# Kernel optimization log

Measured on AMD Instinct MI355X. Metric: run time of the kernel, lower is better.

The kernel has to match this reference:

```python
import jax, jax.numpy as jnp
import numpy as np

N_NODES = 50000
N_EDGES = 800000
IN_CH, OUT_CH, HEADS = 64, 32, 4
NEG_SLOPE = 0.2
BN_EPS = 1e-5


def setup_inputs() -> dict:
    key = jax.random.key(0)
    ks = jax.random.split(key, 9)
    x = jax.random.normal(ks[0], (N_NODES, IN_CH), dtype=jnp.float32)
    pos = jax.random.uniform(ks[1], (N_NODES, 3), dtype=jnp.float32)
    edge_index = jax.random.randint(ks[2], (2, N_EDGES), 0, N_NODES, dtype=jnp.int64)
    s = 1.0 / np.sqrt(IN_CH)
    W_l = jax.random.normal(ks[3], (IN_CH, HEADS * OUT_CH), dtype=jnp.float32) * s
    W_r = jax.random.normal(ks[4], (IN_CH, HEADS * OUT_CH), dtype=jnp.float32) * s
    W_edge = jax.random.normal(ks[5], (3, HEADS * OUT_CH), dtype=jnp.float32) * 0.5
    att = jax.random.normal(ks[6], (HEADS, OUT_CH), dtype=jnp.float32) * (1.0 / np.sqrt(OUT_CH))
    bn_gamma = jax.random.uniform(ks[7], (HEADS * OUT_CH,), dtype=jnp.float32, minval=0.5, maxval=1.5)
    bn_beta = jax.random.normal(ks[8], (HEADS * OUT_CH,), dtype=jnp.float32) * 0.1
    return {"x": x, "pos": pos, "edge_index": edge_index, "W_l": W_l, "W_r": W_r,
            "W_edge": W_edge, "att": att, "bn_gamma": bn_gamma, "bn_beta": bn_beta}


def reference(x, pos, edge_index, W_l, W_r, W_edge, att, bn_gamma, bn_beta):
    N = x.shape[0]
    H, C = att.shape
    # source->target projections (GATv2: lin_l for source/messages, lin_r for target)
    xl = (x @ W_l).reshape(N, H, C)
    xr = (x @ W_r).reshape(N, H, C)
    src, dst = edge_index[0], edge_index[1]
    edge_attr = pos[src] - pos[dst]  # [E,3] relative position as edge feature
    # add self-loops with fill_value='mean' (PyG default)
    loop = jnp.arange(N)
    src = jnp.concatenate([src, loop])
    dst = jnp.concatenate([dst, loop])
    mean_attr = edge_attr.mean(axis=0, keepdims=True)  # [1,3]
    edge_attr = jnp.concatenate([edge_attr, jnp.broadcast_to(mean_attr, (N, 3))], axis=0)
    # per-edge GATv2 score: att . LeakyReLU(x_l[j] + x_r[i] + W_e e_ij)
    e_feat = (edge_attr @ W_edge).reshape(-1, H, C)
    msg = xl[src]                              # [Et,H,C] (reused for aggregation)
    e = msg + xr[dst] + e_feat
    e = jax.nn.leaky_relu(e, NEG_SLOPE)
    score = jnp.einsum('ehc,hc->eh', e, att)   # [Et,H]
    # segment softmax over destination node
    m = jax.ops.segment_max(score, dst, num_segments=N)
    score = jnp.exp(score - m[dst])
    denom = jax.ops.segment_sum(score, dst, num_segments=N)
    alpha = score / (denom[dst] + 1e-16)       # [Et,H]
    out = jax.ops.segment_sum(alpha[:, :, None] * msg, dst, num_segments=N)
    out = out.reshape(N, H * C)
    # BatchNorm over node dimension (training-mode batch statistics, PyG BatchNorm)
    mu = out.mean(axis=0)
    var = out.var(axis=0)
    return (out - mu) / jnp.sqrt(var + BN_EPS) * bn_gamma + bn_beta
```

## Files before the change

kernel.cpp:

```cpp
#include <hip/hip_runtime.h>
#include <hip/hip_bf16.h>

#define N_NODES 50000
#define IN_CH 64
#define HC 128
#define CAP 64
#define NEG_SLOPE 0.2f
#define BN_EPS 1e-5f


__global__ __launch_bounds__(256) void k_gemm(const float* __restrict__ x,
                                              const float* __restrict__ Wl,
                                              const float* __restrict__ Wr,
                                              unsigned int* __restrict__ xl_bf,
                                              float* __restrict__ xr_out,
                                              int* __restrict__ deg,
                                              float* __restrict__ mean_sums,
                                              float* __restrict__ bn_sums,
                                              int* __restrict__ flag,
                                              const int* __restrict__ eidx) {
  {
    int gtid = blockIdx.x * 256 + threadIdx.x;
    if (gtid < N_NODES) deg[gtid] = 1;
    if (gtid < 256) bn_sums[gtid] = 0.f;
    if (gtid < 3) mean_sums[gtid] = 0.f;
    if (blockIdx.x == 0 && threadIdx.x < 64) {
      int w = eidx[2 * threadIdx.x + 1];
      unsigned long long nz = __ballot(w != 0);
      if (threadIdx.x == 0) flag[0] = (nz == 0ULL) ? 1 : 0;
    }
  }

  __shared__ float xs[16][IN_CH];
  __shared__ __hip_bfloat162 wsm[IN_CH][128];
  const int t = threadIdx.x;
  const int row0 = blockIdx.x * 16;

  for (int i = 0; i < 32; ++i) {
    int k = i * 2 + (t >> 7);
    int p = t & 127;
    int cc = p * 2;
    float2 wv;
    if (cc < 128) wv = *(const float2*)(Wl + k * 128 + cc);
    else          wv = *(const float2*)(Wr + k * 128 + (cc - 128));
    wsm[k][p] = __float22bfloat162_rn(wv);
  }
  {
    int r = t >> 4, c4 = (t & 15) * 4;
    *(float4*)&xs[r][c4] = *(const float4*)(x + (row0 + r) * IN_CH + c4);
  }
  __syncthreads();

  const int ct = t & 63;
  const int rt = t >> 6;
  const int c4 = ct * 4;
  const int r4 = rt * 4;

  float acc[4][4];
  #pragma unroll
  for (int a = 0; a < 4; ++a)
    #pragma unroll
    for (int b = 0; b < 4; ++b) acc[a][b] = 0.f;

  #pragma unroll 8
  for (int k = 0; k < IN_CH; ++k) {
    uint2 wraw = *(const uint2*)&wsm[k][ct * 2];
    float2 f01 = __bfloat1622float2(*(__hip_bfloat162*)&wraw.x);
    float2 f23 = __bfloat1622float2(*(__hip_bfloat162*)&wraw.y);
    float wv[4] = {f01.x, f01.y, f23.x, f23.y};
    float xv[4] = {xs[r4][k], xs[r4 + 1][k], xs[r4 + 2][k], xs[r4 + 3][k]};
    #pragma unroll
    for (int a = 0; a < 4; ++a)
      #pragma unroll
      for (int b = 0; b < 4; ++b) acc[a][b] = fmaf(xv[a], wv[b], acc[a][b]);
  }

  #pragma unroll
  for (int a = 0; a < 4; ++a) {
    int row = row0 + r4 + a;
    if (c4 < 128) {
      __hip_bfloat162 b01 = __float22bfloat162_rn(make_float2(acc[a][0], acc[a][1]));
      __hip_bfloat162 b23 = __float22bfloat162_rn(make_float2(acc[a][2], acc[a][3]));
      uint2 u;
      u.x = *(unsigned int*)&b01;
      u.y = *(unsigned int*)&b23;
      *(uint2*)(xl_bf + row * 64 + (c4 >> 1)) = u;
    } else {
      float4 v = make_float4(acc[a][0], acc[a][1], acc[a][2], acc[a][3]);
      *(float4*)(xr_out + row * HC + (c4 - 128)) = v;
    }
  }
}

__global__ __launch_bounds__(256) void k_edges(const int* __restrict__ eidx,
                                               const float* __restrict__ pos,
                                               int* __restrict__ deg,
                                               int* __restrict__ srcs,
                                               float* __restrict__ mean_sums,
                                               const int* __restrict__ flag,
                                               int E) {
  const bool w64 = flag[0] != 0;
  const int tid = blockIdx.x * 256 + threadIdx.x;
  const int base = tid * 8;
  float sx = 0.f, sy = 0.f, sz = 0.f;

  const bool vec_ok = w64 ? ((E & 1) == 0) : ((E & 3) == 0);

  if (base + 8 <= E && vec_ok) {
    int s[8], d[8];
    if (w64) {
      const int4* ps = (const int4*)(eidx + 2 * base);
      int4 A = ps[0], B = ps[1], C = ps[2], D = ps[3];
      s[0]=A.x; s[1]=A.z; s[2]=B.x; s[3]=B.z; s[4]=C.x; s[5]=C.z; s[6]=D.x; s[7]=D.z;
      const int4* pd = (const int4*)(eidx + 2 * E + 2 * base);
      A = pd[0]; B = pd[1]; C = pd[2]; D = pd[3];
      d[0]=A.x; d[1]=A.z; d[2]=B.x; d[3]=B.z; d[4]=C.x; d[5]=C.z; d[6]=D.x; d[7]=D.z;
    } else {
      int4 A = *(const int4*)(eidx + base);
      int4 B = *(const int4*)(eidx + base + 4);
      s[0]=A.x; s[1]=A.y; s[2]=A.z; s[3]=A.w; s[4]=B.x; s[5]=B.y; s[6]=B.z; s[7]=B.w;
      A = *(const int4*)(eidx + E + base);
      B = *(const int4*)(eidx + E + base + 4);
      d[0]=A.x; d[1]=A.y; d[2]=A.z; d[3]=A.w; d[4]=B.x; d[5]=B.y; d[6]=B.z; d[7]=B.w;
    }
    int slot[8];
    #pragma unroll
    for (int k = 0; k < 8; ++k) slot[k] = atomicAdd(&deg[d[k]], 1);
    #pragma unroll
    for (int k = 0; k < 8; ++k)
      if (slot[k] < CAP) srcs[d[k] * CAP + slot[k]] = s[k];
    #pragma unroll
    for (int k = 0; k < 8; ++k) {
      sx += pos[3 * s[k]]     - pos[3 * d[k]];
      sy += pos[3 * s[k] + 1] - pos[3 * d[k] + 1];
      sz += pos[3 * s[k] + 2] - pos[3 * d[k] + 2];
    }
  } else if (base < E) {
    int hi = min(base + 8, E);
    for (int e = base; e < hi; ++e) {
      int s, d;
      if (w64) { s = eidx[2 * e]; d = eidx[2 * (E + e)]; }
      else     { s = eidx[e];     d = eidx[E + e]; }
      int o = atomicAdd(&deg[d], 1);
      if (o < CAP) srcs[d * CAP + o] = s;
      sx += pos[3 * s]     - pos[3 * d];
      sy += pos[3 * s + 1] - pos[3 * d + 1];
      sz += pos[3 * s + 2] - pos[3 * d + 2];
    }
  }

  #pragma unroll
  for (int m = 1; m < 64; m <<= 1) {
    sx += __shfl_xor(sx, m); sy += __shfl_xor(sy, m); sz += __shfl_xor(sz, m);
  }
  __shared__ float red[4][3];
  int wave = threadIdx.x >> 6, lane = threadIdx.x & 63;
  if (lane == 0) { red[wave][0] = sx; red[wave][1] = sy; red[wave][2] = sz; }
  __syncthreads();
  if (threadIdx.x == 0) {
    float a = 0.f, b = 0.f, c = 0.f;
    for (int w = 0; w < 4; ++w) { a += red[w][0]; b += red[w][1]; c += red[w][2]; }
    unsafeAtomicAdd(&mean_sums[0], a);
    unsafeAtomicAdd(&mean_sums[1], b);
    unsafeAtomicAdd(&mean_sums[2], c);
  }
}

__device__ __forceinline__ void edge4(int s, float dx, float dy, float dz, bool valid,
                                      const unsigned int* __restrict__ xl_bf, int l5,
                                      float4 xr4, float4 at4, float4 w0, float4 w1, float4 w2,
                                      float& a0, float& a1, float& a2, float& a3, float& den) {
  uint2 raw = *(const uint2*)(xl_bf + (s << 6) + (l5 << 1));
  float2 x01 = __bfloat1622float2(*(__hip_bfloat162*)&raw.x);
  float2 x23 = __bfloat1622float2(*(__hip_bfloat162*)&raw.y);
  float t0 = x01.x + xr4.x; t0 = fmaf(dx, w0.x, t0); t0 = fmaf(dy, w1.x, t0); t0 = fmaf(dz, w2.x, t0);
  float t1 = x01.y + xr4.y; t1 = fmaf(dx, w0.y, t1); t1 = fmaf(dy, w1.y, t1); t1 = fmaf(dz, w2.y, t1);
  float t2 = x23.x + xr4.z; t2 = fmaf(dx, w0.z, t2); t2 = fmaf(dy, w1.z, t2); t2 = fmaf(dz, w2.z, t2);
  float t3 = x23.y + xr4.w; t3 = fmaf(dx, w0.w, t3); t3 = fmaf(dy, w1.w, t3); t3 = fmaf(dz, w2.w, t3);
  float l0 = fmaf(NEG_SLOPE, fminf(t0, 0.f), fmaxf(t0, 0.f));
  float l1 = fmaf(NEG_SLOPE, fminf(t1, 0.f), fmaxf(t1, 0.f));
  float l2 = fmaf(NEG_SLOPE, fminf(t2, 0.f), fmaxf(t2, 0.f));
  float l3 = fmaf(NEG_SLOPE, fminf(t3, 0.f), fmaxf(t3, 0.f));
  float sc = l0 * at4.x;
  sc = fmaf(l1, at4.y, sc); sc = fmaf(l2, at4.z, sc); sc = fmaf(l3, at4.w, sc);
  sc += __shfl_xor(sc, 1); sc += __shfl_xor(sc, 2); sc += __shfl_xor(sc, 4);
  float e = __expf(sc);
  float p = valid ? e : 0.f;
  den += p;
  a0 = fmaf(p, x01.x, a0); a1 = fmaf(p, x01.y, a1);
  a2 = fmaf(p, x23.x, a2); a3 = fmaf(p, x23.y, a3);
}

__global__ __launch_bounds__(256) void k_agg(const unsigned int* __restrict__ xl_bf,
                                             float* __restrict__ xr_out,
                                             const float* __restrict__ pos,
                                             const float* __restrict__ att,
                                             const float* __restrict__ We,
                                             const float* __restrict__ mean_sums,
                                             const int* __restrict__ srcs,
                                             const int* __restrict__ deg,
                                             float invE) {
  const int lane = threadIdx.x & 63;
  const int half = lane >> 5;
  const int l5 = lane & 31;
  const int c = l5 << 2;

  const float4 at4 = *(const float4*)(att + c);
  const float4 w0 = *(const float4*)(We + c);
  const float4 w1 = *(const float4*)(We + 128 + c);
  const float4 w2 = *(const float4*)(We + 256 + c);
  const float m0 = mean_sums[0] * invE;
  const float m1 = mean_sums[1] * invE;
  const float m2 = mean_sums[2] * invE;

  const int gw = blockIdx.x * 4 + (threadIdx.x >> 6);
  const int W = gridDim.x * 4;

  for (int i = gw; i < N_NODES; i += W) {
    const float4 xr4 = *(const float4*)(xr_out + i * HC + c);
    const float px = pos[3 * i], py = pos[3 * i + 1], pz = pos[3 * i + 2];
    const int di = min(deg[i], CAP);
    const int sreg = srcs[i * CAP + lane];
    float a0 = 0.f, a1 = 0.f, a2 = 0.f, a3 = 0.f, den = 0.f;

    {
      int sA = __shfl(sreg, 1);
      if (half == 0) sA = i;
      bool vA = half < di;
      if (!vA) sA = i;
      int jB = 2 + half;
      int sB = __shfl(sreg, jB);
      bool vB = jB < di;
      if (!vB) sB = i;
      float pax = pos[3 * sA], pay = pos[3 * sA + 1], paz = pos[3 * sA + 2];
      float pbx = pos[3 * sB], pby = pos[3 * sB + 1], pbz = pos[3 * sB + 2];
      float dxA = (half == 0) ? m0 : pax - px;
      float dyA = (half == 0) ? m1 : pay - py;
      float dzA = (half == 0) ? m2 : paz - pz;
      edge4(sA, dxA, dyA, dzA, vA, xl_bf, l5, xr4, at4, w0, w1, w2, a0, a1, a2, a3, den);
      edge4(sB, pbx - px, pby - py, pbz - pz, vB, xl_bf, l5, xr4, at4, w0, w1, w2, a0, a1, a2, a3, den);
    }

    for (int j = 4; j < di; j += 4) {
      int jA = j + half;
      int jB = j + 2 + half;
      int sA = __shfl(sreg, jA);
      int sB = __shfl(sreg, jB);
      bool vA = jA < di;
      bool vB = jB < di;
      if (!vA) sA = i;
      if (!vB) sB = i;
      float pax = pos[3 * sA], pay = pos[3 * sA + 1], paz = pos[3 * sA + 2];
      float pbx = pos[3 * sB], pby = pos[3 * sB + 1], pbz = pos[3 * sB + 2];
      edge4(sA, pax - px, pay - py, paz - pz, vA, xl_bf, l5, xr4, at4, w0, w1, w2, a0, a1, a2, a3, den);
      edge4(sB, pbx - px, pby - py, pbz - pz, vB, xl_bf, l5, xr4, at4, w0, w1, w2, a0, a1, a2, a3, den);
    }

    den += __shfl_xor(den, 32);
    a0 += __shfl_xor(a0, 32);
    a1 += __shfl_xor(a1, 32);
    a2 += __shfl_xor(a2, 32);
    a3 += __shfl_xor(a3, 32);

    float inv = 1.f / (den + 1e-16f);
    if (half == 0) {
      float4 o = make_float4(a0 * inv, a1 * inv, a2 * inv, a3 * inv);
      *(float4*)(xr_out + i * HC + c) = o;
    }
  }
}

__global__ __launch_bounds__(128) void k_bnstats(const float* __restrict__ out,
                                                 float* __restrict__ bn_sums) {
  int c = threadIdx.x;
  float s = 0.f, ss = 0.f;
  int r = blockIdx.x;
  const int g = gridDim.x;
  for (; r + g < N_NODES; r += 2 * g) {
    float v0 = out[r * HC + c];
    float v1 = out[(r + g) * HC + c];
    s += v0; ss = fmaf(v0, v0, ss);
    s += v1; ss = fmaf(v1, v1, ss);
  }
  if (r < N_NODES) {
    float v = out[r * HC + c];
    s += v; ss = fmaf(v, v, ss);
  }
  unsafeAtomicAdd(&bn_sums[c], s);
  unsafeAtomicAdd(&bn_sums[128 + c], ss);
}

__global__ __launch_bounds__(256) void k_bnapply(float* __restrict__ out,
                                                 const float* __restrict__ bn_sums,
                                                 const float* __restrict__ gamma,
                                                 const float* __restrict__ beta,
                                                 int n4) {
  const int stride = gridDim.x * blockDim.x;
  const float invN = 1.f / (float)N_NODES;
  for (int i = blockIdx.x * blockDim.x + threadIdx.x; i < n4; i += stride) {
    int c = (i & 31) * 4;
    float4 v = ((float4*)out)[i];
    float4 s = *(const float4*)(bn_sums + c);
    float4 q = *(const float4*)(bn_sums + 128 + c);
    float4 g = *(const float4*)(gamma + c);
    float4 b = *(const float4*)(beta + c);
    float mu, var, rstd;
    mu = s.x * invN; var = q.x * invN - mu * mu; rstd = rsqrtf(var + BN_EPS);
    v.x = (v.x - mu) * rstd * g.x + b.x;
    mu = s.y * invN; var = q.y * invN - mu * mu; rstd = rsqrtf(var + BN_EPS);
    v.y = (v.y - mu) * rstd * g.y + b.y;
    mu = s.z * invN; var = q.z * invN - mu * mu; rstd = rsqrtf(var + BN_EPS);
    v.z = (v.z - mu) * rstd * g.z + b.z;
    mu = s.w * invN; var = q.w * invN - mu * mu; rstd = rsqrtf(var + BN_EPS);
    v.w = (v.w - mu) * rstd * g.w + b.w;
    ((float4*)out)[i] = v;
  }
}

extern "C" void kernel_launch(void* const* d_in, const int* in_sizes, int n_in,
                              void* d_out, int out_size, void* d_ws, size_t ws_size,
                              hipStream_t stream) {
  const float* x     = (const float*)d_in[0];
  const float* pos   = (const float*)d_in[1];
  const int*   eidx  = (const int*)d_in[2];
  const float* Wl    = (const float*)d_in[3];
  const float* Wr    = (const float*)d_in[4];
  const float* We    = (const float*)d_in[5];
  const float* att   = (const float*)d_in[6];
  const float* gamma = (const float*)d_in[7];
  const float* beta  = (const float*)d_in[8];
  float* out = (float*)d_out;
  const int E = in_sizes[2] / 2;

  char* ws = (char*)d_ws;
  int*   flag      = (int*)(ws + 0);
  float* mean_sums = (float*)(ws + 64);
  float* bn_sums   = (float*)(ws + 1024);
  int*   deg       = (int*)(ws + 4096);
  int*   srcs      = (int*)(ws + (1 << 19));
  unsigned int* xl_bf = (unsigned int*)(ws + (1 << 24));

  k_gemm<<<N_NODES / 16, 256, 0, stream>>>(x, Wl, Wr, xl_bf, out,
                                           deg, mean_sums, bn_sums, flag, eidx);
  int eblocks = (E + 2047) / 2048;
  k_edges<<<eblocks, 256, 0, stream>>>(eidx, pos, deg, srcs, mean_sums, flag, E);
  k_agg<<<2048, 256, 0, stream>>>(xl_bf, out, pos, att, We, mean_sums, srcs, deg,
                                  1.f / (float)E);
  k_bnstats<<<512, 128, 0, stream>>>(out, bn_sums);
  k_bnapply<<<512, 256, 0, stream>>>(out, bn_sums, gamma, beta, out_size / 4);
}
```

Before: 256.6 us.

## Fuse BatchNorm statistics into aggregation and widen per-lane channel tile

Aggregation now assigns 8 channels per lane (16 lanes per edge, 4 edges per step) with 16-byte bf16 gathers instead of two 4-channel edge groups per half-wave. Per-node outputs are also accumulated into shared-memory BatchNorm sum and sum-of-squares buffers, flushed with one global atomic per channel per block. This removes the separate stats kernel and its full re-read of the output. The cost is shared-memory atomics per node and more register pressure from the 8-wide arrays.

After: 277.5 us. 8.2% more time.

```diff
diff --git a/kernel.cpp b/kernel.cpp
--- a/kernel.cpp
+++ b/kernel.cpp
@@ -166,31 +166,6 @@
   }
 }
 
-__device__ __forceinline__ void edge4(int s, float dx, float dy, float dz, bool valid,
-                                      const unsigned int* __restrict__ xl_bf, int l5,
-                                      float4 xr4, float4 at4, float4 w0, float4 w1, float4 w2,
-                                      float& a0, float& a1, float& a2, float& a3, float& den) {
-  uint2 raw = *(const uint2*)(xl_bf + (s << 6) + (l5 << 1));
-  float2 x01 = __bfloat1622float2(*(__hip_bfloat162*)&raw.x);
-  float2 x23 = __bfloat1622float2(*(__hip_bfloat162*)&raw.y);
-  float t0 = x01.x + xr4.x; t0 = fmaf(dx, w0.x, t0); t0 = fmaf(dy, w1.x, t0); t0 = fmaf(dz, w2.x, t0);
-  float t1 = x01.y + xr4.y; t1 = fmaf(dx, w0.y, t1); t1 = fmaf(dy, w1.y, t1); t1 = fmaf(dz, w2.y, t1);
-  float t2 = x23.x + xr4.z; t2 = fmaf(dx, w0.z, t2); t2 = fmaf(dy, w1.z, t2); t2 = fmaf(dz, w2.z, t2);
-  float t3 = x23.y + xr4.w; t3 = fmaf(dx, w0.w, t3); t3 = fmaf(dy, w1.w, t3); t3 = fmaf(dz, w2.w, t3);
-  float l0 = fmaf(NEG_SLOPE, fminf(t0, 0.f), fmaxf(t0, 0.f));
-  float l1 = fmaf(NEG_SLOPE, fminf(t1, 0.f), fmaxf(t1, 0.f));
-  float l2 = fmaf(NEG_SLOPE, fminf(t2, 0.f), fmaxf(t2, 0.f));
-  float l3 = fmaf(NEG_SLOPE, fminf(t3, 0.f), fmaxf(t3, 0.f));
-  float sc = l0 * at4.x;
-  sc = fmaf(l1, at4.y, sc); sc = fmaf(l2, at4.z, sc); sc = fmaf(l3, at4.w, sc);
-  sc += __shfl_xor(sc, 1); sc += __shfl_xor(sc, 2); sc += __shfl_xor(sc, 4);
-  float e = __expf(sc);
-  float p = valid ? e : 0.f;
-  den += p;
-  a0 = fmaf(p, x01.x, a0); a1 = fmaf(p, x01.y, a1);
-  a2 = fmaf(p, x23.x, a2); a3 = fmaf(p, x23.y, a3);
-}
-
 __global__ __launch_bounds__(256) void k_agg(const unsigned int* __restrict__ xl_bf,
                                              float* __restrict__ xr_out,
                                              const float* __restrict__ pos,
@@ -199,16 +174,29 @@
                                              const float* __restrict__ mean_sums,
                                              const int* __restrict__ srcs,
                                              const int* __restrict__ deg,
+                                             float* __restrict__ bn_sums,
                                              float invE) {
+  __shared__ float bnloc[256];
+  bnloc[threadIdx.x] = 0.f;
+  __syncthreads();
+
   const int lane = threadIdx.x & 63;
-  const int half = lane >> 5;
-  const int l5 = lane & 31;
-  const int c = l5 << 2;
-
-  const float4 at4 = *(const float4*)(att + c);
-  const float4 w0 = *(const float4*)(We + c);
-  const float4 w1 = *(const float4*)(We + 128 + c);
-  const float4 w2 = *(const float4*)(We + 256 + c);
+  const int q = lane >> 4;
+  const int l4 = lane & 15;
+  const int c = l4 << 3;
+
+  float at8[8], w08[8], w18[8], w28[8];
+  {
+    float4 A, B;
+    A = *(const float4*)(att + c);        B = *(const float4*)(att + c + 4);
+    at8[0]=A.x; at8[1]=A.y; at8[2]=A.z; at8[3]=A.w; at8[4]=B.x; at8[5]=B.y; at8[6]=B.z; at8[7]=B.w;
+    A = *(const float4*)(We + c);         B = *(const float4*)(We + c + 4);
+    w08[0]=A.x; w08[1]=A.y; w08[2]=A.z; w08[3]=A.w; w08[4]=B.x; w08[5]=B.y; w08[6]=B.z; w08[7]=B.w;
+    A = *(const float4*)(We + 128 + c);   B = *(const float4*)(We + 132 + c);
+    w18[0]=A.x; w18[1]=A.y; w18[2]=A.z; w18[3]=A.w; w18[4]=B.x; w18[5]=B.y; w18[6]=B.z; w18[7]=B.w;
+    A = *(const float4*)(We + 256 + c);   B = *(const float4*)(We + 260 + c);
+    w28[0]=A.x; w28[1]=A.y; w28[2]=A.z; w28[3]=A.w; w28[4]=B.x; w28[5]=B.y; w28[6]=B.z; w28[7]=B.w;
+  }
   const float m0 = mean_sums[0] * invE;
   const float m1 = mean_sums[1] * invE;
   const float m2 = mean_sums[2] * invE;
@@ -217,77 +205,88 @@
   const int W = gridDim.x * 4;
 
   for (int i = gw; i < N_NODES; i += W) {
-    const float4 xr4 = *(const float4*)(xr_out + i * HC + c);
+    float xr8[8];
+    {
+      float4 A = *(const float4*)(xr_out + i * HC + c);
+      float4 B = *(const float4*)(xr_out + i * HC + c + 4);
+      xr8[0]=A.x; xr8[1]=A.y; xr8[2]=A.z; xr8[3]=A.w; xr8[4]=B.x; xr8[5]=B.y; xr8[6]=B.z; xr8[7]=B.w;
+    }
     const float px = pos[3 * i], py = pos[3 * i + 1], pz = pos[3 * i + 2];
     const int di = min(deg[i], CAP);
     const int sreg = srcs[i * CAP + lane];
-    float a0 = 0.f, a1 = 0.f, a2 = 0.f, a3 = 0.f, den = 0.f;
+    float a8[8] = {0.f, 0.f, 0.f, 0.f, 0.f, 0.f, 0.f, 0.f};
+    float den = 0.f;
+
+    auto edge = [&](int s, float dx, float dy, float dz, bool valid) {
+      uint4 raw = *(const uint4*)(xl_bf + (s << 6) + (l4 << 2));
+      float xv[8];
+      float2 f;
+      f = __bfloat1622float2(*(__hip_bfloat162*)&raw.x); xv[0] = f.x; xv[1] = f.y;
+      f = __bfloat1622float2(*(__hip_bfloat162*)&raw.y); xv[2] = f.x; xv[3] = f.y;
+      f = __bfloat1622float2(*(__hip_bfloat162*)&raw.z); xv[4] = f.x; xv[5] = f.y;
+      f = __bfloat1622float2(*(__hip_bfloat162*)&raw.w); xv[6] = f.x; xv[7] = f.y;
+      float sc = 0.f;
+      #pragma unroll
+      for (int k = 0; k < 8; ++k) {
+        float t = xv[k] + xr8[k];
+        t = fmaf(dx, w08[k], t);
+        t = fmaf(dy, w18[k], t);
+        t = fmaf(dz, w28[k], t);
+        float l = fmaf(NEG_SLOPE, fminf(t, 0.f), fmaxf(t, 0.f));
+        sc = fmaf(l, at8[k], sc);
+      }
+      sc += __shfl_xor(sc, 1);
+      sc += __shfl_xor(sc, 2);
+      float p = valid ? __expf(sc) : 0.f;
+      den += p;
+      #pragma unroll
+      for (int k = 0; k < 8; ++k) a8[k] = fmaf(p, xv[k], a8[k]);
+    };
 
     {
-      int sA = __shfl(sreg, 1);
-      if (half == 0) sA = i;
-      bool vA = half < di;
+      int sA = __shfl(sreg, q);
+      bool vA = q < di;
+      if (q == 0 || !vA) sA = i;
+      float pax = pos[3 * sA], pay = pos[3 * sA + 1], paz = pos[3 * sA + 2];
+      float dx = (q == 0) ? m0 : pax - px;
+      float dy = (q == 0) ? m1 : pay - py;
+      float dz = (q == 0) ? m2 : paz - pz;
+      edge(sA, dx, dy, dz, vA);
+    }
+
+    for (int j = 4; j < di; j += 4) {
+      int jA = j + q;
+      int sA = __shfl(sreg, jA);
+      bool vA = jA < di;
       if (!vA) sA = i;
-      int jB = 2 + half;
-      int sB = __shfl(sreg, jB);
-      bool vB = jB < di;
-      if (!vB) sB = i;
       float pax = pos[3 * sA], pay = pos[3 * sA + 1], paz = pos[3 * sA + 2];
-      float pbx = pos[3 * sB], pby = pos[3 * sB + 1], pbz = pos[3 * sB + 2];
-      float dxA = (half == 0) ? m0 : pax - px;
-      float dyA = (half == 0) ? m1 : pay - py;
-      float dzA = (half == 0) ? m2 : paz - pz;
-      edge4(sA, dxA, dyA, dzA, vA, xl_bf, l5, xr4, at4, w0, w1, w2, a0, a1, a2, a3, den);
-      edge4(sB, pbx - px, pby - py, pbz - pz, vB, xl_bf, l5, xr4, at4, w0, w1, w2, a0, a1, a2, a3, den);
-    }
-
-    for (int j = 4; j < di; j += 4) {
-      int jA = j + half;
-      int jB = j + 2 + half;
-      int sA = __shfl(sreg, jA);
-      int sB = __shfl(sreg, jB);
-      bool vA = jA < di;
-      bool vB = jB < di;
-      if (!vA) sA = i;
-      if (!vB) sB = i;
-      float pax = pos[3 * sA], pay = pos[3 * sA + 1], paz = pos[3 * sA + 2];
-      float pbx = pos[3 * sB], pby = pos[3 * sB + 1], pbz = pos[3 * sB + 2];
-      edge4(sA, pax - px, pay - py, paz - pz, vA, xl_bf, l5, xr4, at4, w0, w1, w2, a0, a1, a2, a3, den);
-      edge4(sB, pbx - px, pby - py, pbz - pz, vB, xl_bf, l5, xr4, at4, w0, w1, w2, a0, a1, a2, a3, den);
-    }
-
-    den += __shfl_xor(den, 32);
-    a0 += __shfl_xor(a0, 32);
-    a1 += __shfl_xor(a1, 32);
-    a2 += __shfl_xor(a2, 32);
-    a3 += __shfl_xor(a3, 32);
+      edge(sA, pax - px, pay - py, paz - pz, vA);
+    }
+
+    den += __shfl_xor(den, 16); den += __shfl_xor(den, 32);
+    #pragma unroll
+    for (int k = 0; k < 8; ++k) {
+      a8[k] += __shfl_xor(a8[k], 16);
+      a8[k] += __shfl_xor(a8[k], 32);
+    }
 
     float inv = 1.f / (den + 1e-16f);
-    if (half == 0) {
-      float4 o = make_float4(a0 * inv, a1 * inv, a2 * inv, a3 * inv);
-      *(float4*)(xr_out + i * HC + c) = o;
-    }
-  }
-}
-
-__global__ __launch_bounds__(128) void k_bnstats(const float* __restrict__ out,
-                                                 float* __restrict__ bn_sums) {
-  int c = threadIdx.x;
-  float s = 0.f, ss = 0.f;
-  int r = blockIdx.x;
-  const int g = gridDim.x;
-  for (; r + g < N_NODES; r += 2 * g) {
-    float v0 = out[r * HC + c];
-    float v1 = out[(r + g) * HC + c];
-    s += v0; ss = fmaf(v0, v0, ss);
-    s += v1; ss = fmaf(v1, v1, ss);
-  }
-  if (r < N_NODES) {
-    float v = out[r * HC + c];
-    s += v; ss = fmaf(v, v, ss);
-  }
-  unsafeAtomicAdd(&bn_sums[c], s);
-  unsafeAtomicAdd(&bn_sums[128 + c], ss);
+    if (q == 0) {
+      float o[8];
+      #pragma unroll
+      for (int k = 0; k < 8; ++k) o[k] = a8[k] * inv;
+      *(float4*)(xr_out + i * HC + c)     = make_float4(o[0], o[1], o[2], o[3]);
+      *(float4*)(xr_out + i * HC + c + 4) = make_float4(o[4], o[5], o[6], o[7]);
+      #pragma unroll
+      for (int k = 0; k < 8; ++k) {
+        atomicAdd(&bnloc[c + k], o[k]);
+        atomicAdd(&bnloc[128 + c + k], o[k] * o[k]);
+      }
+    }
+  }
+
+  __syncthreads();
+  unsafeAtomicAdd(&bn_sums[threadIdx.x], bnloc[threadIdx.x]);
 }
 
 __global__ __launch_bounds__(256) void k_bnapply(float* __restrict__ out,
@@ -345,7 +344,6 @@
   int eblocks = (E + 2047) / 2048;
   k_edges<<<eblocks, 256, 0, stream>>>(eidx, pos, deg, srcs, mean_sums, flag, E);
   k_agg<<<2048, 256, 0, stream>>>(xl_bf, out, pos, att, We, mean_sums, srcs, deg,
-                                  1.f / (float)E);
-  k_bnstats<<<512, 128, 0, stream>>>(out, bn_sums);
+                                  bn_sums, 1.f / (float)E);
   k_bnapply<<<512, 256, 0, stream>>>(out, bn_sums, gamma, beta, out_size / 4);
 }
```
